# Performance work log

Hardware: AMD Instinct MI355X
Metric: run time of the kernel (lower is better)

Reference implementation:

```python
import jax, jax.numpy as jnp
import numpy as np

D, H, C = 256, 512, 128  # input_size, hidden_size, num_classes


def setup_inputs() -> dict:
    key = jax.random.key(0)
    ks = jax.random.split(key, 10)
    s_in = 1.0 / np.sqrt(H)  # torch Linear init scale (out_features=H)
    inp = {
        "x": jax.random.normal(ks[0], (512, 64, D), dtype=jnp.float32),
        "h0": jnp.zeros((2, 64, H), dtype=jnp.float32),
        "c0": jnp.zeros((2, 64, H), dtype=jnp.float32),
        # gate order along 4H axis: i, f, o, c
        "W0": jax.random.uniform(ks[1], (4 * H, D), jnp.float32, -s_in, s_in),
        "U0": jax.random.uniform(ks[2], (4 * H, H), jnp.float32, -s_in, s_in),
        "b0": jax.random.uniform(ks[3], (4 * H,), jnp.float32, -s_in, s_in),
        "W1": jax.random.uniform(ks[4], (4 * H, H), jnp.float32, -s_in, s_in),
        "U1": jax.random.uniform(ks[5], (4 * H, H), jnp.float32, -s_in, s_in),
        "b1": jax.random.uniform(ks[6], (4 * H,), jnp.float32, -s_in, s_in),
        "fc_w": jax.random.uniform(ks[7], (C, H), jnp.float32, -s_in, s_in),
        "fc_b": jax.random.uniform(ks[8], (C,), jnp.float32, -s_in, s_in),
    }
    return inp


def _cell(xt, h, c, W, U, b):
    # fused gate projection: equivalent to 8 separate Linears (W_*, U_*) concatenated
    g = xt @ W.T + h @ U.T + b  # [N, 4H]
    i, f, o, ct = jnp.split(g, 4, axis=-1)
    i = jax.nn.sigmoid(i)
    f = jax.nn.sigmoid(f)
    o = jax.nn.sigmoid(o)
    ct = jnp.tanh(ct)
    c_new = f * c + i * ct
    h_new = o * jnp.tanh(c_new)
    return h_new, c_new


def reference(x, h0, c0, W0, U0, b0, W1, U1, b1, fc_w, fc_b):
    def step(carry, xt):
        h_a, c_a, h_b, c_b = carry
        h_a, c_a = _cell(xt, h_a, c_a, W0, U0, b0)
        h_b, c_b = _cell(h_a, h_b, c_b, W1, U1, b1)
        return (h_a, c_a, h_b, c_b), h_b

    carry0 = (h0[0], c0[0], h0[1], c0[1])
    (h_a, c_a, h_b, c_b), out_seq = jax.lax.scan(step, carry0, x)
    out = out_seq[-1] @ fc_w.T + fc_b  # last time step -> [N, C]
    h_n = jnp.stack([h_a, h_b])
    c_n = jnp.stack([c_a, c_b])
    return out, h_n, c_n
```

## Files before the change

### kernel.cpp

```cpp
#include <hip/hip_runtime.h>
#include <hip/hip_fp16.h>

typedef _Float16 f16;
typedef _Float16 f16x8 __attribute__((ext_vector_type(8)));
typedef float f32x4 __attribute__((ext_vector_type(4)));

#define TT 512

#define XH_OFF    0
#define WP_OFF    16777216
#define HA_OFF    24117248
#define HB_OFF    24379392
#define BAR_OFF   24510464
#define WS_NEED   24510976

#define WP_L1_HOFF 1572864
#define LDS_BYTES 131072

#define WAITV(N) do { \
    asm volatile("s_waitcnt vmcnt(" #N ")" ::: "memory"); \
    __builtin_amdgcn_sched_barrier(0); \
  } while (0)


__global__ void k_pack_w(const float* __restrict__ W0, const float* __restrict__ U0,
                         const float* __restrict__ W1, const float* __restrict__ U1,
                         f16* __restrict__ wp) {
  int idx = blockIdx.x * 256 + threadIdx.x;
  if (idx >= 458752) return;
  if (idx < 196608) {
    int w = idx / 6144, r = idx % 6144;
    int ct = r / 1536, r2 = r % 1536;
    int s = r2 / 64, lane = r2 % 64;
    int g = ct * 512 + w * 16 + (lane & 15);
    int kb = s * 32 + (lane >> 4) * 8;
    f16* dst = wp + (size_t)idx * 8;
#pragma unroll
    for (int j = 0; j < 8; ++j) {
      int k = kb + j;
      float v = (k < 256) ? W0[g * 256 + k] : U0[g * 512 + (k - 256)];
      dst[j] = (f16)v;
    }
  } else {
    int i2 = idx - 196608;
    int w = i2 / 8192, r = i2 % 8192;
    int ct = r / 2048, r2 = r % 2048;
    int s = r2 / 64, lane = r2 % 64;
    int g = ct * 512 + w * 16 + (lane & 15);
    int kb = s * 32 + (lane >> 4) * 8;
    f16* dst = wp + (size_t)WP_L1_HOFF + (size_t)i2 * 8;
#pragma unroll
    for (int j = 0; j < 8; ++j) {
      int k = kb + j;
      float v = (k < 512) ? W1[g * 512 + k] : U1[g * 512 + (k - 512)];
      dst[j] = (f16)v;
    }
  }
}

__global__ void k_pack_x(const float* __restrict__ x, f16* __restrict__ xh) {
  int t = blockIdx.x * 256 + threadIdx.x;
  if (t >= 1048576) return;
  const float4* s = (const float4*)(x) + (size_t)t * 2;
  float4 a = s[0], b = s[1];
  f16x8 o;
  o[0] = (f16)a.x; o[1] = (f16)a.y; o[2] = (f16)a.z; o[3] = (f16)a.w;
  o[4] = (f16)b.x; o[5] = (f16)b.y; o[6] = (f16)b.z; o[7] = (f16)b.w;
  *(f16x8*)(xh + (size_t)t * 8) = o;
}

__global__ void k_init(const float* __restrict__ h0, f16* __restrict__ ha,
                       f16* __restrict__ hb, int* __restrict__ slots) {
  int i = blockIdx.x * 256 + threadIdx.x;
  if (i < 32768) {
    ha[i] = (f16)h0[i];
  } else if (i < 65536) {
    hb[i] = (f16)h0[i];
  }
  if (i < 66) slots[i] = 0;
}


__device__ __forceinline__ float sigmoidf_(float x) {
  return 1.0f / (1.0f + __expf(-x));
}
__device__ __forceinline__ float tanhf_(float x) {
  x = fminf(fmaxf(x, -15.0f), 15.0f);
  float e = __expf(-2.0f * x);
  return (1.0f - e) / (1.0f + e);
}

__device__ __forceinline__ uint4 ldg_coh(const void* base, unsigned voff) {
  uint4 d;
  asm volatile("global_load_dwordx4 %0, %1, %2 sc0 sc1"
               : "=v"(d) : "v"(voff), "s"(base) : "memory");
  return d;
}
__device__ __forceinline__ uint4 ldg_x(const void* base, unsigned voff) {
  uint4 d;
  asm volatile("global_load_dwordx4 %0, %1, %2"
               : "=v"(d) : "v"(voff), "s"(base) : "memory");
  return d;
}


template <int LAYER>
__device__ void lstm_body(const f16* __restrict__ xh, const f16* __restrict__ wp,
                          f16* __restrict__ ha, f16* __restrict__ hb,
                          int* __restrict__ slots, const float* __restrict__ c0,
                          const float* __restrict__ bb, float* __restrict__ dout,
                          f16* lds) {
  constexpr int NX = (LAYER == 0) ? 8 : 0;
  constexpr int NH = (LAYER == 0) ? 16 : 32;
  constexpr int NK = NX + NH;
  const int wg = blockIdx.x;
  const int w = wg & 31;
  const int tid = threadIdx.x, lane = tid & 63, wv = tid >> 6;
  int* gens = slots + 64;

  {
    const uint4* src = (const uint4*)(wp + (LAYER ? (size_t)WP_L1_HOFF + (size_t)w * 65536
                                                  : (size_t)w * 49152));
    uint4* dst = (uint4*)lds;
    const int n16 = LAYER ? 8192 : 6144;
    for (int i = tid; i < n16; i += 256) dst[i] = src[i];
  }

  const int j15 = lane & 15;
  const int l4 = lane >> 4;
  const int hidb = w * 16 + j15;
  const float bi = bb[hidb], bf = bb[512 + hidb], bo = bb[1024 + hidb], bc = bb[1536 + hidb];

  float cr[4];
#pragma unroll
  for (int r = 0; r < 4; ++r) {
    int n = 16 * wv + l4 * 4 + r;
    cr[r] = c0[(size_t)LAYER * 32768 + n * 512 + hidb];
  }

  const int row = 16 * wv + j15;
  const unsigned hoffs = (unsigned)(row * 1024 + l4 * 16);
  const unsigned xoffs = (unsigned)(row * 512 + l4 * 16);

  uint4 ax[(LAYER == 0) ? 8 : 1];
  uint4 ah[NH];

  auto issue_x = [&](int pp) {
    if constexpr (LAYER == 0) {
      const char* xb = (const char*)xh + (size_t)pp * 32768;
#pragma unroll
      for (int s = 0; s < 8; ++s) ax[s] = ldg_x(xb, xoffs + s * 64);
    }
  };

  __syncthreads();
  issue_x(0);

  bool broken = false;
  for (int p = 0; p <= TT; ++p) {
    const char* hard = (const char*)ha + (size_t)(p & 3) * 65536;
    const char* hbrd = (const char*)hb + (size_t)(p & 1) * 65536;
    f16* hwr = (LAYER == 0) ? (ha + ((p + 1) & 3) * 32768)
                            : (hb + (((p & 1) ^ 1) * 32768));
    const bool active = (LAYER == 0) ? (p < TT) : (p >= 1);

    if (active) {
      f32x4 acc[4];
#pragma unroll
      for (int ct = 0; ct < 4; ++ct) acc[ct] = (f32x4){0.f, 0.f, 0.f, 0.f};

      auto mstep = [&](uint4 Au, int sB) {
        f16x8 a = __builtin_bit_cast(f16x8, Au);
#pragma unroll
        for (int ct = 0; ct < 4; ++ct) {
          f16x8 b = *(const f16x8*)(lds + (((ct * NK + sB) * 64 + lane) * 8));
          acc[ct] = __builtin_amdgcn_mfma_f32_16x16x32_f16(a, b, acc[ct], 0, 0, 0);
        }
      };

      if constexpr (LAYER == 0) {
#pragma unroll
        for (int t = 0; t < 16; ++t) ah[t] = ldg_coh(hard, hoffs + t * 64);
        WAITV(16);
#pragma unroll
        for (int s = 0; s < 8; ++s) mstep(ax[s], s);
        WAITV(8);
#pragma unroll
        for (int t = 0; t < 8; ++t) mstep(ah[t], 8 + t);
        WAITV(0);
#pragma unroll
        for (int t = 8; t < 16; ++t) mstep(ah[t], 8 + t);
      } else {
#pragma unroll
        for (int t = 0; t < 16; ++t) ah[t] = ldg_coh(hard, hoffs + t * 64);
        WAITV(8);
#pragma unroll
        for (int t = 0; t < 8; ++t) mstep(ah[t], t);
#pragma unroll
        for (int t = 16; t < 24; ++t) ah[t] = ldg_coh(hbrd, hoffs + (t - 16) * 64);
        WAITV(8);
#pragma unroll
        for (int t = 8; t < 16; ++t) mstep(ah[t], t);
#pragma unroll
        for (int t = 24; t < 32; ++t) ah[t] = ldg_coh(hbrd, hoffs + (t - 16) * 64);
        WAITV(8);
#pragma unroll
        for (int t = 16; t < 24; ++t) mstep(ah[t], t);
        WAITV(0);
#pragma unroll
        for (int t = 24; t < 32; ++t) mstep(ah[t], t);
      }

      const bool last = (p == (LAYER ? TT : TT - 1));
#pragma unroll
      for (int r = 0; r < 4; ++r) {
        int n = 16 * wv + l4 * 4 + r;
        float gi = acc[0][r] + bi;
        float gf = acc[1][r] + bf;
        float go = acc[2][r] + bo;
        float gc = acc[3][r] + bc;
        float ig = sigmoidf_(gi), fg = sigmoidf_(gf), og = sigmoidf_(go);
        float cg = tanhf_(gc);
        float c = fg * cr[r] + ig * cg;
        cr[r] = c;
        float h = og * tanhf_(c);
        unsigned short us = __builtin_bit_cast(unsigned short, (f16)h);
        unsigned other = __shfl_xor((unsigned)us, 1, 64);
        if (!(lane & 1)) {
          unsigned pack = (unsigned)us | (other << 16);
          __hip_atomic_store((unsigned*)(hwr + n * 512 + hidb), pack,
                             __ATOMIC_RELAXED, __HIP_MEMORY_SCOPE_AGENT);
        }
        if (last) {
          dout[8192 + LAYER * 32768 + n * 512 + hidb] = h;
          dout[73728 + LAYER * 32768 + n * 512 + hidb] = c;
        }
      }
    }

    WAITV(0);
    __builtin_amdgcn_s_barrier();
    if (tid == 0)
      __hip_atomic_store(slots + wg, p + 1, __ATOMIC_RELAXED, __HIP_MEMORY_SCOPE_AGENT);
    if constexpr (LAYER == 0) {
      if (p + 1 < TT) issue_x(p + 1);
    }
    if (p < TT && wv == 0 && !broken) {
      const int tgt = p + 1;
      if (w == 0) {
        const int* gs = slots + (LAYER ? 32 : 0);
        unsigned spins = 0;
        for (;;) {
          int v = __hip_atomic_load(gs + (lane & 31), __ATOMIC_RELAXED,
                                    __HIP_MEMORY_SCOPE_AGENT);
          if (__all((int)(v >= tgt))) break;
          __builtin_amdgcn_s_sleep(1);
          if (++spins > (1u << 20)) { broken = true; break; }
        }
        __hip_atomic_store(gens + LAYER, tgt, __ATOMIC_RELAXED, __HIP_MEMORY_SCOPE_AGENT);
        const int needO = LAYER ? tgt : (p - 1);
        if (needO > 0 && !broken) {
          spins = 0;
          for (;;) {
            int o = __hip_atomic_load(gens + (1 - LAYER), __ATOMIC_RELAXED,
                                      __HIP_MEMORY_SCOPE_AGENT);
            if (o >= needO) break;
            __builtin_amdgcn_s_sleep(2);
            if (++spins > (1u << 20)) { broken = true; break; }
          }
        }
      } else {
        const int need1 = LAYER ? tgt : (p - 1);
        unsigned spins = 0;
        for (;;) {
          unsigned long long g = __hip_atomic_load((const unsigned long long*)gens,
                                                   __ATOMIC_RELAXED,
                                                   __HIP_MEMORY_SCOPE_AGENT);
          int g0 = (int)(unsigned)g, g1 = (int)(unsigned)(g >> 32);
          if (g0 >= tgt && g1 >= need1) break;
          __builtin_amdgcn_s_sleep(2);
          if (++spins > (1u << 20)) { broken = true; break; }
        }
      }
    }
    __builtin_amdgcn_s_barrier();
  }
}

__global__ __launch_bounds__(256, 1) void k_lstm(const f16* __restrict__ xh,
                                                 const f16* __restrict__ wp,
                                                 f16* __restrict__ ha, f16* __restrict__ hb,
                                                 int* __restrict__ slots,
                                                 const float* __restrict__ c0,
                                                 const float* __restrict__ b0,
                                                 const float* __restrict__ b1,
                                                 float* __restrict__ dout) {
  extern __shared__ f16 lds[];
  if (blockIdx.x < 32) lstm_body<0>(xh, wp, ha, hb, slots, c0, b0, dout, lds);
  else                 lstm_body<1>(xh, wp, ha, hb, slots, c0, b1, dout, lds);
}


__global__ void k_fc(const float* __restrict__ hn1, const float* __restrict__ fcw,
                     const float* __restrict__ fcb, float* __restrict__ out) {
  int n = blockIdx.x, cc = threadIdx.x;
  const float* h = hn1 + n * 512;
  const float* wr = fcw + cc * 512;
  float s = fcb[cc];
#pragma unroll 4
  for (int k = 0; k < 512; k += 4) {
    float4 hv = *(const float4*)(h + k);
    float4 wv = *(const float4*)(wr + k);
    s += hv.x * wv.x + hv.y * wv.y + hv.z * wv.z + hv.w * wv.w;
  }
  out[n * 128 + cc] = s;
}


extern "C" void kernel_launch(void* const* d_in, const int* in_sizes, int n_in,
                              void* d_out, int out_size, void* d_ws, size_t ws_size,
                              hipStream_t stream) {
  const float* x   = (const float*)d_in[0];
  const float* h0  = (const float*)d_in[1];
  const float* c0  = (const float*)d_in[2];
  const float* W0  = (const float*)d_in[3];
  const float* U0  = (const float*)d_in[4];
  const float* b0  = (const float*)d_in[5];
  const float* W1  = (const float*)d_in[6];
  const float* U1  = (const float*)d_in[7];
  const float* b1  = (const float*)d_in[8];
  const float* fcw = (const float*)d_in[9];
  const float* fcb = (const float*)d_in[10];
  float* out = (float*)d_out;
  char* ws = (char*)d_ws;
  if (ws_size < (size_t)WS_NEED) return;

  f16* xh = (f16*)(ws + XH_OFF);
  f16* wp = (f16*)(ws + WP_OFF);
  f16* ha = (f16*)(ws + HA_OFF);
  f16* hb = (f16*)(ws + HB_OFF);
  int* slots = (int*)(ws + BAR_OFF);

  (void)hipFuncSetAttribute((const void*)k_lstm,
                            hipFuncAttributeMaxDynamicSharedMemorySize, LDS_BYTES);

  k_pack_w<<<(458752 + 255) / 256, 256, 0, stream>>>(W0, U0, W1, U1, wp);
  k_pack_x<<<(1048576 + 255) / 256, 256, 0, stream>>>(x, xh);
  k_init<<<256, 256, 0, stream>>>(h0, ha, hb, slots);
  k_lstm<<<64, 256, LDS_BYTES, stream>>>(xh, wp, ha, hb, slots, c0, b0, b1, out);
  k_fc<<<64, 128, 0, stream>>>(out + 8192 + 32768, fcw, fcb, out);
}
```

Measured before the change: 3.673 ms.

## Split layer-1 barrier into two phases and prefetch next layer-0 h early

Layer-1 blocks now wait only for layer-0's generation counter, then immediately issue loads of the next layer-0 hidden state before waiting for their own layer's peers. This overlaps the h_a load latency with the intra-layer barrier. The hb loads are issued all at once at the start of the step. Sleep intervals are also shortened. The protocol is restructured per layer, which raises the risk of races or deadlock in the ring-buffer indexing.

```diff
diff --git a/kernel.cpp b/kernel.cpp
--- a/kernel.cpp
+++ b/kernel.cpp
@@ -157,6 +157,8 @@
   issue_x(0);
 
   bool broken = false;
+
+
   for (int p = 0; p <= TT; ++p) {
     const char* hard = (const char*)ha + (size_t)(p & 3) * 65536;
     const char* hbrd = (const char*)hb + (size_t)(p & 1) * 65536;
@@ -192,17 +194,13 @@
         for (int t = 8; t < 16; ++t) mstep(ah[t], 8 + t);
       } else {
 #pragma unroll
-        for (int t = 0; t < 16; ++t) ah[t] = ldg_coh(hard, hoffs + t * 64);
-        WAITV(8);
+        for (int t = 0; t < 16; ++t) ah[16 + t] = ldg_coh(hbrd, hoffs + t * 64);
+        WAITV(24);
 #pragma unroll
         for (int t = 0; t < 8; ++t) mstep(ah[t], t);
-#pragma unroll
-        for (int t = 16; t < 24; ++t) ah[t] = ldg_coh(hbrd, hoffs + (t - 16) * 64);
-        WAITV(8);
+        WAITV(16);
 #pragma unroll
         for (int t = 8; t < 16; ++t) mstep(ah[t], t);
-#pragma unroll
-        for (int t = 24; t < 32; ++t) ah[t] = ldg_coh(hbrd, hoffs + (t - 16) * 64);
         WAITV(8);
 #pragma unroll
         for (int t = 16; t < 24; ++t) mstep(ah[t], t);
@@ -238,52 +236,88 @@
       }
     }
 
-    WAITV(0);
-    __builtin_amdgcn_s_barrier();
-    if (tid == 0)
-      __hip_atomic_store(slots + wg, p + 1, __ATOMIC_RELAXED, __HIP_MEMORY_SCOPE_AGENT);
-    if constexpr (LAYER == 0) {
-      if (p + 1 < TT) issue_x(p + 1);
-    }
-    if (p < TT && wv == 0 && !broken) {
+    if (p < TT) {
       const int tgt = p + 1;
-      if (w == 0) {
-        const int* gs = slots + (LAYER ? 32 : 0);
-        unsigned spins = 0;
-        for (;;) {
-          int v = __hip_atomic_load(gs + (lane & 31), __ATOMIC_RELAXED,
-                                    __HIP_MEMORY_SCOPE_AGENT);
-          if (__all((int)(v >= tgt))) break;
-          __builtin_amdgcn_s_sleep(1);
-          if (++spins > (1u << 20)) { broken = true; break; }
-        }
-        __hip_atomic_store(gens + LAYER, tgt, __ATOMIC_RELAXED, __HIP_MEMORY_SCOPE_AGENT);
-        const int needO = LAYER ? tgt : (p - 1);
-        if (needO > 0 && !broken) {
-          spins = 0;
-          for (;;) {
-            int o = __hip_atomic_load(gens + (1 - LAYER), __ATOMIC_RELAXED,
-                                      __HIP_MEMORY_SCOPE_AGENT);
-            if (o >= needO) break;
-            __builtin_amdgcn_s_sleep(2);
+      WAITV(0);
+      __builtin_amdgcn_s_barrier();
+      if (tid == 0)
+        __hip_atomic_store(slots + wg, tgt, __ATOMIC_RELAXED,
+                           __HIP_MEMORY_SCOPE_AGENT);
+
+      if constexpr (LAYER == 0) {
+        if (p + 1 < TT) issue_x(p + 1);
+        if (wv == 0 && !broken) {
+          if (w == 0) {
+            const int* gs = slots;
+            unsigned spins = 0;
+            for (;;) {
+              int v = __hip_atomic_load(gs + (lane & 31), __ATOMIC_RELAXED,
+                                        __HIP_MEMORY_SCOPE_AGENT);
+              if (__all((int)(v >= tgt))) break;
+              __builtin_amdgcn_s_sleep(1);
+              if (++spins > (1u << 20)) { broken = true; break; }
+            }
+            __hip_atomic_store(gens + 0, tgt, __ATOMIC_RELAXED,
+                               __HIP_MEMORY_SCOPE_AGENT);
+            const int needO = p - 1;
+            if (needO > 0 && !broken) {
+              unsigned s2 = 0;
+              while (__hip_atomic_load(gens + 1, __ATOMIC_RELAXED,
+                                       __HIP_MEMORY_SCOPE_AGENT) < needO) {
+                __builtin_amdgcn_s_sleep(1);
+                if (++s2 > (1u << 20)) { broken = true; break; }
+              }
+            }
+          } else {
+            unsigned spins = 0;
+            while (__hip_atomic_load(gens + 0, __ATOMIC_RELAXED,
+                                     __HIP_MEMORY_SCOPE_AGENT) < tgt) {
+              __builtin_amdgcn_s_sleep(1);
+              if (++spins > (1u << 20)) { broken = true; break; }
+            }
+          }
+        }
+        __builtin_amdgcn_s_barrier();
+      } else {
+        if (wv == 0 && !broken) {
+          unsigned spins = 0;
+          while (__hip_atomic_load(gens + 0, __ATOMIC_RELAXED,
+                                   __HIP_MEMORY_SCOPE_AGENT) < tgt) {
+            __builtin_amdgcn_s_sleep(1);
             if (++spins > (1u << 20)) { broken = true; break; }
           }
         }
-      } else {
-        const int need1 = LAYER ? tgt : (p - 1);
-        unsigned spins = 0;
-        for (;;) {
-          unsigned long long g = __hip_atomic_load((const unsigned long long*)gens,
-                                                   __ATOMIC_RELAXED,
-                                                   __HIP_MEMORY_SCOPE_AGENT);
-          int g0 = (int)(unsigned)g, g1 = (int)(unsigned)(g >> 32);
-          if (g0 >= tgt && g1 >= need1) break;
-          __builtin_amdgcn_s_sleep(2);
-          if (++spins > (1u << 20)) { broken = true; break; }
-        }
+        __builtin_amdgcn_s_barrier();
+        {
+          const char* hardN = (const char*)ha + (size_t)(tgt & 3) * 65536;
+#pragma unroll
+          for (int t = 0; t < 16; ++t) ah[t] = ldg_coh(hardN, hoffs + t * 64);
+        }
+        if (wv == 0 && !broken) {
+          if (w == 0) {
+            const int* gs = slots + 32;
+            unsigned spins = 0;
+            for (;;) {
+              int v = __hip_atomic_load(gs + (lane & 31), __ATOMIC_RELAXED,
+                                        __HIP_MEMORY_SCOPE_AGENT);
+              if (__all((int)(v >= tgt))) break;
+              __builtin_amdgcn_s_sleep(1);
+              if (++spins > (1u << 20)) { broken = true; break; }
+            }
+            __hip_atomic_store(gens + 1, tgt, __ATOMIC_RELAXED,
+                               __HIP_MEMORY_SCOPE_AGENT);
+          } else {
+            unsigned spins = 0;
+            while (__hip_atomic_load(gens + 1, __ATOMIC_RELAXED,
+                                     __HIP_MEMORY_SCOPE_AGENT) < tgt) {
+              __builtin_amdgcn_s_sleep(1);
+              if (++spins > (1u << 20)) { broken = true; break; }
+            }
+          }
+        }
+        __builtin_amdgcn_s_barrier();
       }
     }
-    __builtin_amdgcn_s_barrier();
   }
 }
 
```

After: 4.294 ms. +16.9%, slower.
